# Kernel optimization log

Measured on AMD Instinct MI355X. Metric: run time of the kernel, lower is better.

Reference implementation:

```python
import jax, jax.numpy as jnp
import numpy as np
from jax import lax

N_FFT = 512
HOP = 128
Q = N_FFT // HOP  # 4
KW = 2 * N_FFT - 1  # conv kernel width 1023


def _hann_periodic(n: int) -> np.ndarray:
    # scipy.signal.get_window('hann', n) default fftbins=True -> periodic hann
    k = np.arange(n)
    return (0.5 - 0.5 * np.cos(2.0 * np.pi * k / n)).astype(np.float64)


def _compute_alpha(W: np.ndarray, S: np.ndarray) -> np.ndarray:
    # Faithful port of ConsistencyLoss._compute_alpha (paper eq. 9)
    N, R = N_FFT, HOP
    alpha = np.zeros((2 * Q - 1, 2 * N - 1), dtype=np.complex64)
    for qi, q in enumerate(range(-(Q - 1), Q)):
        S_sh = np.zeros(N)
        s0, s1 = max(0, -q * R), min(N, N - q * R)
        if s0 < s1:
            S_sh[s0:s1] = S[q * R + s0: q * R + s1]
        term = W * S_sh
        f = np.fft.fft(term, 2 * N - 1)
        alpha[qi] = np.fft.fftshift(f) / N
    alpha[Q - 1, N - 1] -= 1.0
    return alpha


def setup_inputs() -> dict:
    key = jax.random.key(0)
    waveform = 0.1 * jax.random.normal(key, (4, 131072), dtype=jnp.float32)
    W_np = _hann_periodic(N_FFT)
    alpha = _compute_alpha(W_np, W_np)
    return {
        "waveform": waveform,
        "window": jnp.asarray(W_np, dtype=jnp.float32),
        "alpha_real": jnp.asarray(alpha.real, dtype=jnp.float32),
        "alpha_imag": jnp.asarray(alpha.imag, dtype=jnp.float32),
    }


def _stft(waveform, window):
    # torch.stft(center=True, pad_mode='reflect', onesided=True), output (B, T, F)
    N, hop = N_FFT, HOP
    B, L = waveform.shape
    padded = jnp.pad(waveform, ((0, 0), (N // 2, N // 2)), mode="reflect")
    T = 1 + L // hop
    idx = hop * jnp.arange(T)[:, None] + jnp.arange(N)[None, :]  # (T, N)
    frames = padded[:, idx] * window  # (B, T, N)
    return jnp.fft.rfft(frames, axis=-1)  # (B, T, N//2+1) complex64


def reference(waveform, window, alpha_real, alpha_imag):
    N, hop = N_FFT, HOP
    B = waveform.shape[0]
    H = _stft(waveform, window)  # (B, T, N//2+1)
    T = H.shape[1]

    # reconstruct full two-sided spectrum: concat conj-flipped interior bins
    H_full = jnp.concatenate([H, jnp.conj(H[:, :, 1:-1][:, :, ::-1])], axis=2)  # (B, T, N)
    H_full = jnp.transpose(H_full, (0, 2, 1))  # (B, N, T)

    # fuse the phase-term einsum into the per-frequency conv kernel:
    # C[b,n,t] = sum_q phase[n,q] * (alpha[q] * H_full[b,n])(t)
    #          = (K_eff[n] * H_full[b,n])(t),  K_eff = phase @ alpha
    q_idx = jnp.arange(-(Q - 1), Q, dtype=jnp.float32)
    n_idx = jnp.arange(N, dtype=jnp.float32)
    phase = jnp.exp(1j * (2.0 * jnp.pi / N) * n_idx[:, None] * q_idx[None, :])  # (N, 2Q-1)
    alpha = alpha_real + 1j * alpha_imag  # (2Q-1, KW)
    K = phase @ alpha.astype(jnp.complex64)  # (N, KW)
    Kr, Ki = jnp.real(K), jnp.imag(K)

    # complex depthwise (groups=N) cross-correlation via real 2-channel trick
    Hri = jnp.stack([jnp.real(H_full), jnp.imag(H_full)], axis=2).reshape(B, 2 * N, T)
    kern = jnp.stack([
        jnp.stack([Kr, -Ki], axis=1),  # real output rows (N, 2, KW)
        jnp.stack([Ki, Kr], axis=1),   # imag output rows (N, 2, KW)
    ], axis=1).reshape(2 * N, 2, KW)
    out = lax.conv_general_dilated(
        Hri, kern, window_strides=(1,), padding=[(N - 1, N - 1)],
        dimension_numbers=("NCH", "OIH", "NCH"), feature_group_count=N,
    )  # (B, 2N, T)
    Cr, Ci = out[:, 0::2], out[:, 1::2]  # (B, N, T)

    loss = jnp.sum(Cr * Cr + Ci * Ci)
    return loss / (B * T)
```

## Files before the change

### kernel.cpp

```cpp
#include <hip/hip_runtime.h>
#include <math.h>

#define T_FRAMES 1025
#define TSTRIDE  1032
#define BATCH    4
#define LWAV     131072
#define KWC      1023
#define MFFT     2048
#define PI_F     3.14159265358979323846f

struct c32 { float r, i; };
__device__ __forceinline__ c32 mkc(float r, float i){ c32 z; z.r=r; z.i=i; return z; }
__device__ __forceinline__ c32 cadd(c32 a, c32 b){ return mkc(a.r+b.r, a.i+b.i); }
__device__ __forceinline__ c32 csub(c32 a, c32 b){ return mkc(a.r-b.r, a.i-b.i); }
__device__ __forceinline__ c32 cmul(c32 a, c32 b){ return mkc(a.r*b.r - a.i*b.i, a.r*b.i + a.i*b.r); }
__device__ __forceinline__ c32 cni(c32 a){ return mkc(a.i, -a.r); }
#define C8F 0.70710678118654752440f
__device__ __forceinline__ c32 c8p(c32 a){ return mkc(C8F*(a.r+a.i), C8F*(a.i-a.r)); }
__device__ __forceinline__ c32 c8m(c32 a){ return mkc(C8F*(a.i-a.r), -C8F*(a.r+a.i)); }

__device__ __forceinline__ int pX(int j){ return j + (j >> 5); }
__device__ __forceinline__ int pS(int j){ return j + (j >> 3); }

__device__ __forceinline__ c32 wexp(int r) {
    float s, c;
    __sincosf((float)r * (-PI_F / 1024.0f), &s, &c);
    return mkc(c, s);
}

__device__ __forceinline__ void dif8_tw(c32 y[8], c32 w3) {
    c32 w2 = cmul(w3, w3), w1 = cmul(w2, w2);
    c32 u[8], v[8], d;
    d = csub(y[0], y[4]); u[0] = cadd(y[0], y[4]); u[4] = cmul(d, w3);
    d = csub(y[1], y[5]); u[1] = cadd(y[1], y[5]); u[5] = c8p(cmul(d, w3));
    d = csub(y[2], y[6]); u[2] = cadd(y[2], y[6]); u[6] = cni(cmul(d, w3));
    d = csub(y[3], y[7]); u[3] = cadd(y[3], y[7]); u[7] = c8m(cmul(d, w3));
    d = csub(u[0], u[2]); v[0] = cadd(u[0], u[2]); v[2] = cmul(d, w2);
    d = csub(u[1], u[3]); v[1] = cadd(u[1], u[3]); v[3] = cni(cmul(d, w2));
    d = csub(u[4], u[6]); v[4] = cadd(u[4], u[6]); v[6] = cmul(d, w2);
    d = csub(u[5], u[7]); v[5] = cadd(u[5], u[7]); v[7] = cni(cmul(d, w2));
    d = csub(v[0], v[1]); y[0] = cadd(v[0], v[1]); y[1] = cmul(d, w1);
    d = csub(v[2], v[3]); y[2] = cadd(v[2], v[3]); y[3] = cmul(d, w1);
    d = csub(v[4], v[5]); y[4] = cadd(v[4], v[5]); y[5] = cmul(d, w1);
    d = csub(v[6], v[7]); y[6] = cadd(v[6], v[7]); y[7] = cmul(d, w1);
}
__device__ __forceinline__ void dif8_nt(c32 y[8]) {
    c32 u[8], v[8], d;
    d = csub(y[0], y[4]); u[0] = cadd(y[0], y[4]); u[4] = d;
    d = csub(y[1], y[5]); u[1] = cadd(y[1], y[5]); u[5] = c8p(d);
    d = csub(y[2], y[6]); u[2] = cadd(y[2], y[6]); u[6] = cni(d);
    d = csub(y[3], y[7]); u[3] = cadd(y[3], y[7]); u[7] = c8m(d);
    d = csub(u[0], u[2]); v[0] = cadd(u[0], u[2]); v[2] = d;
    d = csub(u[1], u[3]); v[1] = cadd(u[1], u[3]); v[3] = cni(d);
    d = csub(u[4], u[6]); v[4] = cadd(u[4], u[6]); v[6] = d;
    d = csub(u[5], u[7]); v[5] = cadd(u[5], u[7]); v[7] = cni(d);
    d = csub(v[0], v[1]); y[0] = cadd(v[0], v[1]); y[1] = d;
    d = csub(v[2], v[3]); y[2] = cadd(v[2], v[3]); y[3] = d;
    d = csub(v[4], v[5]); y[4] = cadd(v[4], v[5]); y[5] = d;
    d = csub(v[6], v[7]); y[6] = cadd(v[6], v[7]); y[7] = d;
}
__device__ __forceinline__ void dit8_tw(c32 y[8], c32 w3) {
    c32 w2 = cmul(w3, w3), w1 = cmul(w2, w2);
    c32 u[8], v[8], t;
    t = cmul(y[1], w1); u[0] = cadd(y[0], t); u[1] = csub(y[0], t);
    t = cmul(y[3], w1); u[2] = cadd(y[2], t); u[3] = csub(y[2], t);
    t = cmul(y[5], w1); u[4] = cadd(y[4], t); u[5] = csub(y[4], t);
    t = cmul(y[7], w1); u[6] = cadd(y[6], t); u[7] = csub(y[6], t);
    t = cmul(u[2], w2);      v[0] = cadd(u[0], t); v[2] = csub(u[0], t);
    t = cni(cmul(u[3], w2)); v[1] = cadd(u[1], t); v[3] = csub(u[1], t);
    t = cmul(u[6], w2);      v[4] = cadd(u[4], t); v[6] = csub(u[4], t);
    t = cni(cmul(u[7], w2)); v[5] = cadd(u[5], t); v[7] = csub(u[5], t);
    t = cmul(v[4], w3);      y[0] = cadd(v[0], t); y[4] = csub(v[0], t);
    t = c8p(cmul(v[5], w3)); y[1] = cadd(v[1], t); y[5] = csub(v[1], t);
    t = cni(cmul(v[6], w3)); y[2] = cadd(v[2], t); y[6] = csub(v[2], t);
    t = c8m(cmul(v[7], w3)); y[3] = cadd(v[3], t); y[7] = csub(v[3], t);
}
__device__ __forceinline__ void dit8_nt(c32 y[8]) {
    c32 u[8], v[8], t;
    u[0] = cadd(y[0], y[1]); u[1] = csub(y[0], y[1]);
    u[2] = cadd(y[2], y[3]); u[3] = csub(y[2], y[3]);
    u[4] = cadd(y[4], y[5]); u[5] = csub(y[4], y[5]);
    u[6] = cadd(y[6], y[7]); u[7] = csub(y[6], y[7]);
    t = u[2];      v[0] = cadd(u[0], t); v[2] = csub(u[0], t);
    t = cni(u[3]); v[1] = cadd(u[1], t); v[3] = csub(u[1], t);
    t = u[6];      v[4] = cadd(u[4], t); v[6] = csub(u[4], t);
    t = cni(u[7]); v[5] = cadd(u[5], t); v[7] = csub(u[5], t);
    t = v[4];      y[0] = cadd(v[0], t); y[4] = csub(v[0], t);
    t = c8p(v[5]); y[1] = cadd(v[1], t); y[5] = csub(v[1], t);
    t = cni(v[6]); y[2] = cadd(v[2], t); y[6] = csub(v[2], t);
    t = c8m(v[7]); y[3] = cadd(v[3], t); y[7] = csub(v[3], t);
}
__device__ __forceinline__ void dif4(c32 y[4]) {
    c32 u0 = cadd(y[0], y[2]), d0 = csub(y[0], y[2]);
    c32 u1 = cadd(y[1], y[3]), d1 = cni(csub(y[1], y[3]));
    y[0] = cadd(u0, u1); y[1] = csub(u0, u1);
    y[2] = cadd(d0, d1); y[3] = csub(d0, d1);
}
__device__ __forceinline__ void dit4(c32 y[4], c32 w) {
    c32 w2 = cmul(w, w);
    c32 t1 = cmul(y[1], w2); c32 u0 = cadd(y[0], t1), u1 = csub(y[0], t1);
    c32 t3 = cmul(y[3], w2); c32 u2 = cadd(y[2], t3), u3 = csub(y[2], t3);
    c32 s2 = cmul(u2, w);      y[0] = cadd(u0, s2); y[2] = csub(u0, s2);
    c32 s3 = cni(cmul(u3, w)); y[1] = cadd(u1, s3); y[3] = csub(u1, s3);
}

__global__ __launch_bounds__(256) void stage1_kernel(const float* __restrict__ wave,
                                                     const float* __restrict__ win,
                                                     const float* __restrict__ ar,
                                                     const float* __restrict__ ai,
                                                     float2* __restrict__ Ht,
                                                     float2* __restrict__ Afbr) {
    __shared__ float lds[9216];
    const int tid = threadIdx.x;

    if (blockIdx.x < 516) {
        float* Fr = lds;
        float* Fi = lds + 4608;
        const int w = tid >> 6, l = tid & 63;
        const int b = blockIdx.x / 129;
        const int t0 = (blockIdx.x - b * 129) << 3;
        const float* wb = wave + (size_t)b * LWAV;

        for (int pass = 0; pass < 2; ++pass) {
            const int j = w + (pass << 2);
            const int t = t0 + j;
            if (t < T_FRAMES) {
                c32 y[8];
#pragma unroll
                for (int k = 0; k < 8; ++k) {
                    int s = l + (k << 6);
                    int posn = t * 128 + s - 256;
                    int ix = posn < 0 ? -posn : (posn >= LWAV ? 2 * LWAV - 2 - posn : posn);
                    y[k] = mkc(wb[ix] * win[s], 0.f);
                }
                dif8_tw(y, wexp(l << 2));
#pragma unroll
                for (int k = 0; k < 8; ++k) { int p = pS(l + (k << 6)); Fr[j*576+p] = y[k].r; Fi[j*576+p] = y[k].i; }
                __builtin_amdgcn_wave_barrier();
                {
                    int base = ((l >> 3) << 6) + (l & 7);
#pragma unroll
                    for (int k = 0; k < 8; ++k) { int p = pS(base + (k << 3)); y[k] = mkc(Fr[j*576+p], Fi[j*576+p]); }
                    dif8_tw(y, wexp((l & 7) << 5));
#pragma unroll
                    for (int k = 0; k < 8; ++k) { int p = pS(base + (k << 3)); Fr[j*576+p] = y[k].r; Fi[j*576+p] = y[k].i; }
                }
                __builtin_amdgcn_wave_barrier();
                {
#pragma unroll
                    for (int k = 0; k < 8; ++k) { int p = pS((l << 3) + k); y[k] = mkc(Fr[j*576+p], Fi[j*576+p]); }
                    dif8_nt(y);
#pragma unroll
                    for (int k = 0; k < 8; ++k) { int p = pS((l << 3) + k); Fr[j*576+p] = y[k].r; Fi[j*576+p] = y[k].i; }
                }
            }
        }
        __syncthreads();
        const bool full = (t0 + 7 < T_FRAMES);
#pragma unroll
        for (int h = 0; h < 2; ++h) {
            int p = tid + (h << 8);
            int bin = (int)(__brev((unsigned)p) >> 23);
            if (bin > 256) continue;
            int ps = pS(p);
            size_t rowbase = (size_t)(b * 512 + p) * TSTRIDE + t0;
            if (full) {
                float4* dst = (float4*)(Ht + rowbase);
#pragma unroll
                for (int jj = 0; jj < 4; ++jj)
                    dst[jj] = make_float4(Fr[2*jj*576+ps], Fi[2*jj*576+ps], Fr[(2*jj+1)*576+ps], Fi[(2*jj+1)*576+ps]);
            } else {
                for (int jj = 0; jj < 8; ++jj)
                    if (t0 + jj < T_FRAMES) Ht[rowbase + jj] = make_float2(Fr[jj*576+ps], Fi[jj*576+ps]);
            }
        }
    } else {
        float* Xr = lds;
        float* Xi = lds + 2112;
        const int q = blockIdx.x - 516;
        c32 y[8];
#pragma unroll
        for (int k = 0; k < 8; ++k) {
            int j = tid + (k << 8);
            y[k] = (j < KWC) ? mkc(ar[q * KWC + j], -ai[q * KWC + j]) : mkc(0.f, 0.f);
        }
        dif8_tw(y, wexp(tid));
#pragma unroll
        for (int k = 0; k < 8; ++k) { int p = pX(tid + (k << 8)); Xr[p] = y[k].r; Xi[p] = y[k].i; }
        __syncthreads();
        {
            int base = ((tid >> 5) << 8) + (tid & 31);
#pragma unroll
            for (int k = 0; k < 8; ++k) { int p = pX(base + (k << 5)); y[k] = mkc(Xr[p], Xi[p]); }
            dif8_tw(y, wexp((tid & 31) << 3));
#pragma unroll
            for (int k = 0; k < 8; ++k) { int p = pX(base + (k << 5)); Xr[p] = y[k].r; Xi[p] = y[k].i; }
        }
        __syncthreads();
        {
            int base = ((tid & 63) << 5) + (tid >> 6);
#pragma unroll
            for (int k = 0; k < 8; ++k) { int p = pX(base + (k << 2)); y[k] = mkc(Xr[p], Xi[p]); }
            dif8_tw(y, wexp((tid >> 6) << 6));
#pragma unroll
            for (int k = 0; k < 8; ++k) { int p = pX(base + (k << 2)); Xr[p] = y[k].r; Xi[p] = y[k].i; }
        }
        __syncthreads();
#pragma unroll
        for (int h = 0; h < 2; ++h) {
            int g = tid + (h << 8);
            c32 z4[4];
#pragma unroll
            for (int k = 0; k < 4; ++k) { int p = pX((g << 2) + k); z4[k] = mkc(Xr[p], Xi[p]); }
            dif4(z4);
#pragma unroll
            for (int k = 0; k < 4; ++k) Afbr[(q << 11) + (g << 2) + k] = make_float2(z4[k].r, -z4[k].i);
        }
    }
}

__global__ __launch_bounds__(256) void conv_fft_kernel(const float2* __restrict__ Ht,
                                                       const float2* __restrict__ Afbr,
                                                       float* __restrict__ out) {
    __shared__ float Xr[2112], Xi[2112];
    __shared__ float red[4];
    const int tid = threadIdx.x;
    const int b = blockIdx.x / 257;
    const int n = blockIdx.x - b * 257;
    const int pr = (int)(__brev((unsigned)n) >> 23);

    const float2* row = Ht + (size_t)(b * 512 + pr) * TSTRIDE;
    c32 y[8];
#pragma unroll
    for (int k = 0; k < 8; ++k) {
        int j = tid + (k << 8);
        c32 v = mkc(0.f, 0.f);
        if (j < T_FRAMES) { float2 h = row[j]; v = mkc(h.x, h.y); }
        y[k] = v;
    }
    dif8_tw(y, wexp(tid));
#pragma unroll
    for (int k = 0; k < 8; ++k) { int p = pX(tid + (k << 8)); Xr[p] = y[k].r; Xi[p] = y[k].i; }
    __syncthreads();
    {
        int base = ((tid >> 5) << 8) + (tid & 31);
#pragma unroll
        for (int k = 0; k < 8; ++k) { int p = pX(base + (k << 5)); y[k] = mkc(Xr[p], Xi[p]); }
        dif8_tw(y, wexp((tid & 31) << 3));
#pragma unroll
        for (int k = 0; k < 8; ++k) { int p = pX(base + (k << 5)); Xr[p] = y[k].r; Xi[p] = y[k].i; }
    }
    __syncthreads();
    {
        int base = ((tid & 63) << 5) + (tid >> 6);
#pragma unroll
        for (int k = 0; k < 8; ++k) { int p = pX(base + (k << 2)); y[k] = mkc(Xr[p], Xi[p]); }
        dif8_tw(y, wexp((tid >> 6) << 6));
#pragma unroll
        for (int k = 0; k < 8; ++k) { int p = pX(base + (k << 2)); Xr[p] = y[k].r; Xi[p] = y[k].i; }
    }
    __syncthreads();
    {
        c32 p1 = wexp(-(n << 2));
        c32 p2 = cmul(p1, p1);
        c32 p3 = cmul(p2, p1);
        const int a0 = tid << 3;
        const int p0 = pX(a0);
        c32 z[8];
#pragma unroll
        for (int k = 0; k < 8; ++k) z[k] = mkc(Xr[p0 + k], Xi[p0 + k]);
        dif4(&z[0]);
        dif4(&z[4]);
        const float4* af4 = (const float4*)(Afbr + a0);
#pragma unroll
        for (int k = 0; k < 8; ++k) {
            float4 a;
            c32 Kk;
            a = af4[(3 << 10) + (k >> 1)];
            float ax = (k & 1) ? a.z : a.x, ay = (k & 1) ? a.w : a.y;
            Kk = mkc(ax, ay);
            a = af4[(4 << 10) + (k >> 1)]; ax = (k & 1) ? a.z : a.x; ay = (k & 1) ? a.w : a.y;
            Kk.r += p1.r * ax - p1.i * ay;  Kk.i += p1.r * ay + p1.i * ax;
            a = af4[(2 << 10) + (k >> 1)]; ax = (k & 1) ? a.z : a.x; ay = (k & 1) ? a.w : a.y;
            Kk.r += p1.r * ax + p1.i * ay;  Kk.i += p1.r * ay - p1.i * ax;
            a = af4[(5 << 10) + (k >> 1)]; ax = (k & 1) ? a.z : a.x; ay = (k & 1) ? a.w : a.y;
            Kk.r += p2.r * ax - p2.i * ay;  Kk.i += p2.r * ay + p2.i * ax;
            a = af4[(1 << 10) + (k >> 1)]; ax = (k & 1) ? a.z : a.x; ay = (k & 1) ? a.w : a.y;
            Kk.r += p2.r * ax + p2.i * ay;  Kk.i += p2.r * ay - p2.i * ax;
            a = af4[(6 << 10) + (k >> 1)]; ax = (k & 1) ? a.z : a.x; ay = (k & 1) ? a.w : a.y;
            Kk.r += p3.r * ax - p3.i * ay;  Kk.i += p3.r * ay + p3.i * ax;
            a = af4[(0 << 10) + (k >> 1)]; ax = (k & 1) ? a.z : a.x; ay = (k & 1) ? a.w : a.y;
            Kk.r += p3.r * ax + p3.i * ay;  Kk.i += p3.r * ay - p3.i * ax;
            c32 P = cmul(z[k], Kk);
            z[k] = mkc(P.r, -P.i);
        }
        dit8_nt(z);
#pragma unroll
        for (int k = 0; k < 8; ++k) { Xr[p0 + k] = z[k].r; Xi[p0 + k] = z[k].i; }
    }
    __syncthreads();
    {
        int G = (((tid & 63) >> 3) << 2) + (tid >> 6);
        int pos = tid & 7;
        int base = (G << 6) + pos;
#pragma unroll
        for (int k = 0; k < 8; ++k) { int p = pX(base + (k << 3)); y[k] = mkc(Xr[p], Xi[p]); }
        dit8_tw(y, wexp(pos << 5));
#pragma unroll
        for (int k = 0; k < 8; ++k) { int p = pX(base + (k << 3)); Xr[p] = y[k].r; Xi[p] = y[k].i; }
    }
    __syncthreads();
    {
        int base = ((tid >> 6) << 9) + (tid & 63);
#pragma unroll
        for (int k = 0; k < 8; ++k) { int p = pX(base + (k << 6)); y[k] = mkc(Xr[p], Xi[p]); }
        dit8_tw(y, wexp((tid & 63) << 2));
#pragma unroll
        for (int k = 0; k < 8; ++k) { int p = pX(base + (k << 6)); Xr[p] = y[k].r; Xi[p] = y[k].i; }
    }
    __syncthreads();
    float local = 0.f;
#pragma unroll
    for (int h = 0; h < 2; ++h) {
        int pos = tid + (h << 8);
        c32 z4[4];
#pragma unroll
        for (int k = 0; k < 4; ++k) { int p = pX(pos + (k << 9)); z4[k] = mkc(Xr[p], Xi[p]); }
        dit4(z4, wexp(pos));
        local += z4[0].r * z4[0].r + z4[0].i * z4[0].i;
        if (pos < 2)  local += z4[1].r * z4[1].r + z4[1].i * z4[1].i;
        if (pos >= 1) local += z4[3].r * z4[3].r + z4[3].i * z4[3].i;
    }
    local *= (n == 0 || n == 256) ? 1.0f : 2.0f;
#pragma unroll
    for (int off = 32; off >= 1; off >>= 1) local += __shfl_down(local, off);
    if ((tid & 63) == 0) red[tid >> 6] = local;
    __syncthreads();
    if (tid == 0) {
        const float SCALE =
            (float)(1.0 / ((double)MFFT * (double)MFFT * (double)BATCH * (double)T_FRAMES));
        atomicAdd(out, (red[0] + red[1] + red[2] + red[3]) * SCALE);
    }
}

extern "C" void kernel_launch(void* const* d_in, const int* in_sizes, int n_in,
                              void* d_out, int out_size, void* d_ws, size_t ws_size,
                              hipStream_t stream) {
    (void)in_sizes; (void)n_in; (void)out_size; (void)ws_size;
    const float* wave   = (const float*)d_in[0];
    const float* window = (const float*)d_in[1];
    const float* ar     = (const float*)d_in[2];
    const float* ai     = (const float*)d_in[3];
    float* out = (float*)d_out;

    char* ws = (char*)d_ws;
    float2* Ht   = (float2*)ws;
    float2* Afbr = (float2*)(ws + 16908288);

    hipMemsetAsync(out, 0, sizeof(float), stream);
    stage1_kernel<<<523, 256, 0, stream>>>(wave, window, ar, ai, Ht, Afbr);
    conv_fft_kernel<<<BATCH * 257, 256, 0, stream>>>(Ht, Afbr, out);
}
```

Before: 94.95 us.

## Use radix-4 FFT with 512 threads in conv kernel, halve STFT block size

The 2048-point conv FFT moves from three radix-8 passes with 256 threads to five radix-4 passes with 512 threads, so each thread holds less register state and more threads run per row. The STFT stage processes 4 frames per block instead of 8, doubling the block count, and the output zeroing moves into an extra block of that kernel in place of a separate memset launch. The trade-off is more barriers and shared-memory round trips per FFT in exchange for higher parallelism and one fewer launch.

```diff
diff --git a/kernel.cpp b/kernel.cpp
--- a/kernel.cpp
+++ b/kernel.cpp
@@ -21,6 +21,8 @@
 
 __device__ __forceinline__ int pX(int j){ return j + (j >> 5); }
 __device__ __forceinline__ int pS(int j){ return j + (j >> 3); }
+__device__ __forceinline__ int pP(int j){ return j + (j >> 3); }
+__device__ __forceinline__ int rev9(int j){ return (int)(__brev((unsigned)j) >> 23); }
 
 __device__ __forceinline__ c32 wexp(int r) {
     float s, c;
@@ -59,42 +61,14 @@
     d = csub(v[4], v[5]); y[4] = cadd(v[4], v[5]); y[5] = d;
     d = csub(v[6], v[7]); y[6] = cadd(v[6], v[7]); y[7] = d;
 }
-__device__ __forceinline__ void dit8_tw(c32 y[8], c32 w3) {
-    c32 w2 = cmul(w3, w3), w1 = cmul(w2, w2);
-    c32 u[8], v[8], t;
-    t = cmul(y[1], w1); u[0] = cadd(y[0], t); u[1] = csub(y[0], t);
-    t = cmul(y[3], w1); u[2] = cadd(y[2], t); u[3] = csub(y[2], t);
-    t = cmul(y[5], w1); u[4] = cadd(y[4], t); u[5] = csub(y[4], t);
-    t = cmul(y[7], w1); u[6] = cadd(y[6], t); u[7] = csub(y[6], t);
-    t = cmul(u[2], w2);      v[0] = cadd(u[0], t); v[2] = csub(u[0], t);
-    t = cni(cmul(u[3], w2)); v[1] = cadd(u[1], t); v[3] = csub(u[1], t);
-    t = cmul(u[6], w2);      v[4] = cadd(u[4], t); v[6] = csub(u[4], t);
-    t = cni(cmul(u[7], w2)); v[5] = cadd(u[5], t); v[7] = csub(u[5], t);
-    t = cmul(v[4], w3);      y[0] = cadd(v[0], t); y[4] = csub(v[0], t);
-    t = c8p(cmul(v[5], w3)); y[1] = cadd(v[1], t); y[5] = csub(v[1], t);
-    t = cni(cmul(v[6], w3)); y[2] = cadd(v[2], t); y[6] = csub(v[2], t);
-    t = c8m(cmul(v[7], w3)); y[3] = cadd(v[3], t); y[7] = csub(v[3], t);
-}
-__device__ __forceinline__ void dit8_nt(c32 y[8]) {
-    c32 u[8], v[8], t;
-    u[0] = cadd(y[0], y[1]); u[1] = csub(y[0], y[1]);
-    u[2] = cadd(y[2], y[3]); u[3] = csub(y[2], y[3]);
-    u[4] = cadd(y[4], y[5]); u[5] = csub(y[4], y[5]);
-    u[6] = cadd(y[6], y[7]); u[7] = csub(y[6], y[7]);
-    t = u[2];      v[0] = cadd(u[0], t); v[2] = csub(u[0], t);
-    t = cni(u[3]); v[1] = cadd(u[1], t); v[3] = csub(u[1], t);
-    t = u[6];      v[4] = cadd(u[4], t); v[6] = csub(u[4], t);
-    t = cni(u[7]); v[5] = cadd(u[5], t); v[7] = csub(u[5], t);
-    t = v[4];      y[0] = cadd(v[0], t); y[4] = csub(v[0], t);
-    t = c8p(v[5]); y[1] = cadd(v[1], t); y[5] = csub(v[1], t);
-    t = cni(v[6]); y[2] = cadd(v[2], t); y[6] = csub(v[2], t);
-    t = c8m(v[7]); y[3] = cadd(v[3], t); y[7] = csub(v[3], t);
-}
-__device__ __forceinline__ void dif4(c32 y[4]) {
-    c32 u0 = cadd(y[0], y[2]), d0 = csub(y[0], y[2]);
-    c32 u1 = cadd(y[1], y[3]), d1 = cni(csub(y[1], y[3]));
-    y[0] = cadd(u0, u1); y[1] = csub(u0, u1);
-    y[2] = cadd(d0, d1); y[3] = csub(d0, d1);
+__device__ __forceinline__ void dif4_tw(c32 y[4], c32 w) {
+    c32 w2 = cmul(w, w), w3 = cmul(w2, w);
+    c32 t0 = cadd(y[0], y[2]), t1 = cadd(y[1], y[3]);
+    c32 t2 = csub(y[0], y[2]), t3 = cni(csub(y[1], y[3]));
+    y[0] = cadd(t0, t1);
+    y[1] = cmul(csub(t0, t1), w2);
+    y[2] = cmul(cadd(t2, t3), w);
+    y[3] = cmul(csub(t2, t3), w3);
 }
 __device__ __forceinline__ void dit4(c32 y[4], c32 w) {
     c32 w2 = cmul(w, w);
@@ -103,81 +77,84 @@
     c32 s2 = cmul(u2, w);      y[0] = cadd(u0, s2); y[2] = csub(u0, s2);
     c32 s3 = cni(cmul(u3, w)); y[1] = cadd(u1, s3); y[3] = csub(u1, s3);
 }
+__device__ __forceinline__ void dif4(c32 y[4]) {
+    c32 u0 = cadd(y[0], y[2]), d0 = csub(y[0], y[2]);
+    c32 u1 = cadd(y[1], y[3]), d1 = cni(csub(y[1], y[3]));
+    y[0] = cadd(u0, u1); y[1] = csub(u0, u1);
+    y[2] = cadd(d0, d1); y[3] = csub(d0, d1);
+}
 
 __global__ __launch_bounds__(256) void stage1_kernel(const float* __restrict__ wave,
                                                      const float* __restrict__ win,
                                                      const float* __restrict__ ar,
                                                      const float* __restrict__ ai,
                                                      float2* __restrict__ Ht,
-                                                     float2* __restrict__ Afbr) {
-    __shared__ float lds[9216];
+                                                     float2* __restrict__ Afbr,
+                                                     float* __restrict__ out) {
+    __shared__ float lds[4608];
     const int tid = threadIdx.x;
 
-    if (blockIdx.x < 516) {
+    if (blockIdx.x < 1028) {
         float* Fr = lds;
-        float* Fi = lds + 4608;
+        float* Fi = lds + 2304;
         const int w = tid >> 6, l = tid & 63;
-        const int b = blockIdx.x / 129;
-        const int t0 = (blockIdx.x - b * 129) << 3;
+        const int b = blockIdx.x / 257;
+        const int t0 = (blockIdx.x - b * 257) << 2;
+        const int t = t0 + w;
         const float* wb = wave + (size_t)b * LWAV;
 
-        for (int pass = 0; pass < 2; ++pass) {
-            const int j = w + (pass << 2);
-            const int t = t0 + j;
-            if (t < T_FRAMES) {
-                c32 y[8];
-#pragma unroll
-                for (int k = 0; k < 8; ++k) {
-                    int s = l + (k << 6);
-                    int posn = t * 128 + s - 256;
-                    int ix = posn < 0 ? -posn : (posn >= LWAV ? 2 * LWAV - 2 - posn : posn);
-                    y[k] = mkc(wb[ix] * win[s], 0.f);
-                }
-                dif8_tw(y, wexp(l << 2));
-#pragma unroll
-                for (int k = 0; k < 8; ++k) { int p = pS(l + (k << 6)); Fr[j*576+p] = y[k].r; Fi[j*576+p] = y[k].i; }
-                __builtin_amdgcn_wave_barrier();
-                {
-                    int base = ((l >> 3) << 6) + (l & 7);
-#pragma unroll
-                    for (int k = 0; k < 8; ++k) { int p = pS(base + (k << 3)); y[k] = mkc(Fr[j*576+p], Fi[j*576+p]); }
-                    dif8_tw(y, wexp((l & 7) << 5));
-#pragma unroll
-                    for (int k = 0; k < 8; ++k) { int p = pS(base + (k << 3)); Fr[j*576+p] = y[k].r; Fi[j*576+p] = y[k].i; }
-                }
-                __builtin_amdgcn_wave_barrier();
-                {
-#pragma unroll
-                    for (int k = 0; k < 8; ++k) { int p = pS((l << 3) + k); y[k] = mkc(Fr[j*576+p], Fi[j*576+p]); }
-                    dif8_nt(y);
-#pragma unroll
-                    for (int k = 0; k < 8; ++k) { int p = pS((l << 3) + k); Fr[j*576+p] = y[k].r; Fi[j*576+p] = y[k].i; }
-                }
+        if (t < T_FRAMES) {
+            c32 y[8];
+#pragma unroll
+            for (int k = 0; k < 8; ++k) {
+                int s = l + (k << 6);
+                int posn = t * 128 + s - 256;
+                int ix = posn < 0 ? -posn : (posn >= LWAV ? 2 * LWAV - 2 - posn : posn);
+                y[k] = mkc(wb[ix] * win[s], 0.f);
             }
+            dif8_tw(y, wexp(l << 2));
+#pragma unroll
+            for (int k = 0; k < 8; ++k) { int p = pS(l + (k << 6)); Fr[w*576+p] = y[k].r; Fi[w*576+p] = y[k].i; }
+            __builtin_amdgcn_wave_barrier();
+            {
+                int base = ((l >> 3) << 6) + (l & 7);
+#pragma unroll
+                for (int k = 0; k < 8; ++k) { int p = pS(base + (k << 3)); y[k] = mkc(Fr[w*576+p], Fi[w*576+p]); }
+                dif8_tw(y, wexp((l & 7) << 5));
+#pragma unroll
+                for (int k = 0; k < 8; ++k) { int p = pS(base + (k << 3)); Fr[w*576+p] = y[k].r; Fi[w*576+p] = y[k].i; }
+            }
+            __builtin_amdgcn_wave_barrier();
+            {
+#pragma unroll
+                for (int k = 0; k < 8; ++k) { int p = pS((l << 3) + k); y[k] = mkc(Fr[w*576+p], Fi[w*576+p]); }
+                dif8_nt(y);
+#pragma unroll
+                for (int k = 0; k < 8; ++k) { int p = pS((l << 3) + k); Fr[w*576+p] = y[k].r; Fi[w*576+p] = y[k].i; }
+            }
         }
         __syncthreads();
-        const bool full = (t0 + 7 < T_FRAMES);
+        const bool full = (t0 + 3 < T_FRAMES);
 #pragma unroll
         for (int h = 0; h < 2; ++h) {
             int p = tid + (h << 8);
-            int bin = (int)(__brev((unsigned)p) >> 23);
+            int bin = rev9(p);
             if (bin > 256) continue;
             int ps = pS(p);
             size_t rowbase = (size_t)(b * 512 + p) * TSTRIDE + t0;
             if (full) {
                 float4* dst = (float4*)(Ht + rowbase);
-#pragma unroll
+                dst[0] = make_float4(Fr[0*576+ps], Fi[0*576+ps], Fr[1*576+ps], Fi[1*576+ps]);
+                dst[1] = make_float4(Fr[2*576+ps], Fi[2*576+ps], Fr[3*576+ps], Fi[3*576+ps]);
+            } else {
                 for (int jj = 0; jj < 4; ++jj)
-                    dst[jj] = make_float4(Fr[2*jj*576+ps], Fi[2*jj*576+ps], Fr[(2*jj+1)*576+ps], Fi[(2*jj+1)*576+ps]);
-            } else {
-                for (int jj = 0; jj < 8; ++jj)
                     if (t0 + jj < T_FRAMES) Ht[rowbase + jj] = make_float2(Fr[jj*576+ps], Fi[jj*576+ps]);
             }
         }
-    } else {
+    } else if (blockIdx.x < 1035) {
         float* Xr = lds;
         float* Xi = lds + 2112;
-        const int q = blockIdx.x - 516;
+        const int q = blockIdx.x - 1028;
         c32 y[8];
 #pragma unroll
         for (int k = 0; k < 8; ++k) {
@@ -216,64 +193,87 @@
 #pragma unroll
             for (int k = 0; k < 4; ++k) Afbr[(q << 11) + (g << 2) + k] = make_float2(z4[k].r, -z4[k].i);
         }
-    }
-}
-
-__global__ __launch_bounds__(256) void conv_fft_kernel(const float2* __restrict__ Ht,
-                                                       const float2* __restrict__ Afbr,
-                                                       float* __restrict__ out) {
-    __shared__ float Xr[2112], Xi[2112];
-    __shared__ float red[4];
+    } else {
+        if (tid == 0) *out = 0.f;
+    }
+}
+
+__global__ __launch_bounds__(512) void conv_kernel(const float2* __restrict__ Ht,
+                                                   const float2* __restrict__ Afbr,
+                                                   float* __restrict__ out) {
+    __shared__ float lds[4616];
+    float* Xr = lds;
+    float* Xi = lds + 2304;
+    float* red = lds + 4608;
     const int tid = threadIdx.x;
-    const int b = blockIdx.x / 257;
-    const int n = blockIdx.x - b * 257;
-    const int pr = (int)(__brev((unsigned)n) >> 23);
+    const int r = blockIdx.x;
+    const int b = r / 257;
+    const int n = r - b * 257;
+    const int pr = rev9(n);
 
     const float2* row = Ht + (size_t)(b * 512 + pr) * TSTRIDE;
-    c32 y[8];
-#pragma unroll
-    for (int k = 0; k < 8; ++k) {
-        int j = tid + (k << 8);
+    c32 y[4];
+#pragma unroll
+    for (int k = 0; k < 4; ++k) {
+        int j = tid + (k << 9);
         c32 v = mkc(0.f, 0.f);
         if (j < T_FRAMES) { float2 h = row[j]; v = mkc(h.x, h.y); }
         y[k] = v;
     }
-    dif8_tw(y, wexp(tid));
-#pragma unroll
-    for (int k = 0; k < 8; ++k) { int p = pX(tid + (k << 8)); Xr[p] = y[k].r; Xi[p] = y[k].i; }
-    __syncthreads();
-    {
-        int base = ((tid >> 5) << 8) + (tid & 31);
-#pragma unroll
-        for (int k = 0; k < 8; ++k) { int p = pX(base + (k << 5)); y[k] = mkc(Xr[p], Xi[p]); }
-        dif8_tw(y, wexp((tid & 31) << 3));
-#pragma unroll
-        for (int k = 0; k < 8; ++k) { int p = pX(base + (k << 5)); Xr[p] = y[k].r; Xi[p] = y[k].i; }
-    }
-    __syncthreads();
-    {
-        int base = ((tid & 63) << 5) + (tid >> 6);
-#pragma unroll
-        for (int k = 0; k < 8; ++k) { int p = pX(base + (k << 2)); y[k] = mkc(Xr[p], Xi[p]); }
-        dif8_tw(y, wexp((tid >> 6) << 6));
-#pragma unroll
-        for (int k = 0; k < 8; ++k) { int p = pX(base + (k << 2)); Xr[p] = y[k].r; Xi[p] = y[k].i; }
+    dif4_tw(y, wexp(tid));
+#pragma unroll
+    for (int k = 0; k < 4; ++k) { int p = pP(tid + (k << 9)); Xr[p] = y[k].r; Xi[p] = y[k].i; }
+    __syncthreads();
+    {
+        int base = ((tid >> 7) << 9) + (tid & 127);
+#pragma unroll
+        for (int k = 0; k < 4; ++k) { int p = pP(base + (k << 7)); y[k] = mkc(Xr[p], Xi[p]); }
+        dif4_tw(y, wexp((tid & 127) << 2));
+#pragma unroll
+        for (int k = 0; k < 4; ++k) { int p = pP(base + (k << 7)); Xr[p] = y[k].r; Xi[p] = y[k].i; }
+    }
+    __syncthreads();
+    {
+        int base = ((tid >> 5) << 7) + (tid & 31);
+#pragma unroll
+        for (int k = 0; k < 4; ++k) { int p = pP(base + (k << 5)); y[k] = mkc(Xr[p], Xi[p]); }
+        dif4_tw(y, wexp((tid & 31) << 4));
+#pragma unroll
+        for (int k = 0; k < 4; ++k) { int p = pP(base + (k << 5)); Xr[p] = y[k].r; Xi[p] = y[k].i; }
+    }
+    __syncthreads();
+    {
+        int base = ((tid >> 3) << 5) + (tid & 7);
+#pragma unroll
+        for (int k = 0; k < 4; ++k) { int p = pP(base + (k << 3)); y[k] = mkc(Xr[p], Xi[p]); }
+        dif4_tw(y, wexp((tid & 7) << 6));
+#pragma unroll
+        for (int k = 0; k < 4; ++k) { int p = pP(base + (k << 3)); Xr[p] = y[k].r; Xi[p] = y[k].i; }
+    }
+    __syncthreads();
+    {
+        int base = ((tid >> 1) << 3) + (tid & 1);
+#pragma unroll
+        for (int k = 0; k < 4; ++k) { int p = pP(base + (k << 1)); y[k] = mkc(Xr[p], Xi[p]); }
+        dif4_tw(y, wexp((tid & 1) << 8));
+#pragma unroll
+        for (int k = 0; k < 4; ++k) { int p = pP(base + (k << 1)); Xr[p] = y[k].r; Xi[p] = y[k].i; }
     }
     __syncthreads();
     {
         c32 p1 = wexp(-(n << 2));
         c32 p2 = cmul(p1, p1);
         c32 p3 = cmul(p2, p1);
-        const int a0 = tid << 3;
-        const int p0 = pX(a0);
-        c32 z[8];
-#pragma unroll
-        for (int k = 0; k < 8; ++k) z[k] = mkc(Xr[p0 + k], Xi[p0 + k]);
-        dif4(&z[0]);
-        dif4(&z[4]);
+        const int a0 = tid << 2;
+        const int q0 = pP(a0);
+        c32 z[4];
+#pragma unroll
+        for (int k = 0; k < 4; ++k) z[k] = mkc(Xr[q0 + k], Xi[q0 + k]);
+        { c32 a = z[0], bq = z[1]; z[0] = cadd(a, bq); z[1] = csub(a, bq); }
+        { c32 a = z[2], bq = z[3]; z[2] = cadd(a, bq); z[3] = csub(a, bq); }
         const float4* af4 = (const float4*)(Afbr + a0);
 #pragma unroll
-        for (int k = 0; k < 8; ++k) {
+        for (int k = 0; k < 4; ++k) {
             float4 a;
             c32 Kk;
             a = af4[(3 << 10) + (k >> 1)];
@@ -294,42 +294,56 @@
             c32 P = cmul(z[k], Kk);
             z[k] = mkc(P.r, -P.i);
         }
-        dit8_nt(z);
-#pragma unroll
-        for (int k = 0; k < 8; ++k) { Xr[p0 + k] = z[k].r; Xi[p0 + k] = z[k].i; }
-    }
-    __syncthreads();
-    {
-        int G = (((tid & 63) >> 3) << 2) + (tid >> 6);
-        int pos = tid & 7;
-        int base = (G << 6) + pos;
-#pragma unroll
-        for (int k = 0; k < 8; ++k) { int p = pX(base + (k << 3)); y[k] = mkc(Xr[p], Xi[p]); }
-        dit8_tw(y, wexp(pos << 5));
-#pragma unroll
-        for (int k = 0; k < 8; ++k) { int p = pX(base + (k << 3)); Xr[p] = y[k].r; Xi[p] = y[k].i; }
-    }
-    __syncthreads();
-    {
-        int base = ((tid >> 6) << 9) + (tid & 63);
-#pragma unroll
-        for (int k = 0; k < 8; ++k) { int p = pX(base + (k << 6)); y[k] = mkc(Xr[p], Xi[p]); }
-        dit8_tw(y, wexp((tid & 63) << 2));
-#pragma unroll
-        for (int k = 0; k < 8; ++k) { int p = pX(base + (k << 6)); Xr[p] = y[k].r; Xi[p] = y[k].i; }
+        { c32 a = z[0], bq = z[1]; z[0] = cadd(a, bq); z[1] = csub(a, bq); }
+        { c32 a = z[2], bq = z[3]; z[2] = cadd(a, bq); z[3] = csub(a, bq); }
+#pragma unroll
+        for (int k = 0; k < 4; ++k) { Xr[q0 + k] = z[k].r; Xi[q0 + k] = z[k].i; }
+    }
+    __syncthreads();
+    {
+        int base = ((tid >> 1) << 3) + (tid & 1);
+#pragma unroll
+        for (int k = 0; k < 4; ++k) { int p = pP(base + (k << 1)); y[k] = mkc(Xr[p], Xi[p]); }
+        dit4(y, wexp((tid & 1) << 8));
+#pragma unroll
+        for (int k = 0; k < 4; ++k) { int p = pP(base + (k << 1)); Xr[p] = y[k].r; Xi[p] = y[k].i; }
+    }
+    __syncthreads();
+    {
+        int base = ((tid >> 3) << 5) + (tid & 7);
+#pragma unroll
+        for (int k = 0; k < 4; ++k) { int p = pP(base + (k << 3)); y[k] = mkc(Xr[p], Xi[p]); }
+        dit4(y, wexp((tid & 7) << 6));
+#pragma unroll
+        for (int k = 0; k < 4; ++k) { int p = pP(base + (k << 3)); Xr[p] = y[k].r; Xi[p] = y[k].i; }
+    }
+    __syncthreads();
+    {
+        int base = ((tid >> 5) << 7) + (tid & 31);
+#pragma unroll
+        for (int k = 0; k < 4; ++k) { int p = pP(base + (k << 5)); y[k] = mkc(Xr[p], Xi[p]); }
+        dit4(y, wexp((tid & 31) << 4));
+#pragma unroll
+        for (int k = 0; k < 4; ++k) { int p = pP(base + (k << 5)); Xr[p] = y[k].r; Xi[p] = y[k].i; }
+    }
+    __syncthreads();
+    {
+        int base = ((tid >> 7) << 9) + (tid & 127);
+#pragma unroll
+        for (int k = 0; k < 4; ++k) { int p = pP(base + (k << 7)); y[k] = mkc(Xr[p], Xi[p]); }
+        dit4(y, wexp((tid & 127) << 2));
+#pragma unroll
+        for (int k = 0; k < 4; ++k) { int p = pP(base + (k << 7)); Xr[p] = y[k].r; Xi[p] = y[k].i; }
     }
     __syncthreads();
     float local = 0.f;
-#pragma unroll
-    for (int h = 0; h < 2; ++h) {
-        int pos = tid + (h << 8);
-        c32 z4[4];
-#pragma unroll
-        for (int k = 0; k < 4; ++k) { int p = pX(pos + (k << 9)); z4[k] = mkc(Xr[p], Xi[p]); }
-        dit4(z4, wexp(pos));
-        local += z4[0].r * z4[0].r + z4[0].i * z4[0].i;
-        if (pos < 2)  local += z4[1].r * z4[1].r + z4[1].i * z4[1].i;
-        if (pos >= 1) local += z4[3].r * z4[3].r + z4[3].i * z4[3].i;
+    {
+#pragma unroll
+        for (int k = 0; k < 4; ++k) { int p = pP(tid + (k << 9)); y[k] = mkc(Xr[p], Xi[p]); }
+        dit4(y, wexp(tid));
+        local += y[0].r * y[0].r + y[0].i * y[0].i;
+        if (tid < 2)  local += y[1].r * y[1].r + y[1].i * y[1].i;
+        if (tid >= 1) local += y[3].r * y[3].r + y[3].i * y[3].i;
     }
     local *= (n == 0 || n == 256) ? 1.0f : 2.0f;
 #pragma unroll
@@ -339,7 +353,10 @@
     if (tid == 0) {
         const float SCALE =
             (float)(1.0 / ((double)MFFT * (double)MFFT * (double)BATCH * (double)T_FRAMES));
-        atomicAdd(out, (red[0] + red[1] + red[2] + red[3]) * SCALE);
+        float s = 0.f;
+#pragma unroll
+        for (int i = 0; i < 8; ++i) s += red[i];
+        atomicAdd(out, s * SCALE);
     }
 }
 
@@ -357,7 +374,6 @@
     float2* Ht   = (float2*)ws;
     float2* Afbr = (float2*)(ws + 16908288);
 
-    hipMemsetAsync(out, 0, sizeof(float), stream);
-    stage1_kernel<<<523, 256, 0, stream>>>(wave, window, ar, ai, Ht, Afbr);
-    conv_fft_kernel<<<BATCH * 257, 256, 0, stream>>>(Ht, Afbr, out);
-}
+    stage1_kernel<<<1036, 256, 0, stream>>>(wave, window, ar, ai, Ht, Afbr, out);
+    conv_kernel<<<BATCH * 257, 512, 0, stream>>>(Ht, Afbr, out);
+}
```

Result: no change. 93.56 us (-1.5%).
